# Performance work log

Hardware: AMD Instinct MI355X
Metric: run time of the kernel (lower is better)

## Reference

```python
import jax, jax.numpy as jnp
import numpy as np

IN_DIM = 1024
HID = 1024
DEPTH = 13            # perfect binary tree: 2**13 = 8192 leaves, 8191 internal nodes
N_LEAVES = 2 ** DEPTH
N_TOKENS = 8192
N_OPS = 4             # '+', '/', '*', '-' (ordered_op=False)


def setup_inputs() -> dict:
    key = jax.random.key(0)
    ks = jax.random.split(key, 16)
    sW = 1.0 / np.sqrt(IN_DIM)
    sU = 1.0 / np.sqrt(HID)
    inp = {
        "tokens": jax.random.normal(ks[0], (N_TOKENS, IN_DIM), jnp.float32),
        "leaf_token_ids": jax.random.randint(ks[1], (N_LEAVES,), 0, N_TOKENS),
        "op_ids": jax.random.randint(ks[2], (N_LEAVES - 1,), 0, N_OPS),
        "W_i": jax.random.normal(ks[3], (HID, IN_DIM), jnp.float32) * sW,
        "W_o": jax.random.normal(ks[4], (HID, IN_DIM), jnp.float32) * sW,
        "W_u": jax.random.normal(ks[5], (HID, IN_DIM), jnp.float32) * sW,
        "W_f": jax.random.normal(ks[6], (HID, IN_DIM), jnp.float32) * sW,
        "U_i": jax.random.normal(ks[7], (HID, HID), jnp.float32) * sU,
        "U_o": jax.random.normal(ks[8], (HID, HID), jnp.float32) * sU,
        "U_u": jax.random.normal(ks[9], (HID, HID), jnp.float32) * sU,
        "U_f": jax.random.normal(ks[10], (HID, HID), jnp.float32) * sU,
        "b_i": jnp.zeros((1, HID), jnp.float32),
        "b_o": jnp.zeros((1, HID), jnp.float32),
        "b_u": jnp.zeros((1, HID), jnp.float32),
        "b_f": jnp.zeros((1, HID), jnp.float32),
        "op_emb": jax.random.uniform(ks[11], (N_OPS, IN_DIM), jnp.float32, -1.0, 1.0),
        "c_init": jnp.zeros((2, HID), jnp.float32),
        "h_init": jnp.zeros((2, HID), jnp.float32),
    }
    return inp


def reference(tokens, leaf_token_ids, op_ids, W_i, W_o, W_u, W_f,
              U_i, U_o, U_u, U_f, b_i, b_o, b_u, b_f,
              op_emb, c_init, h_init):
    """Depth-batched Child-Sum TreeLSTM over a perfect binary tree.
    op_ids are stored root-first level order: level l (root=0) occupies
    op_ids[2**l - 1 : 2**(l+1) - 1]. Leaves are level DEPTH.
    Children of node j at level l are nodes 2j, 2j+1 at level l+1.
    Returns jnp.stack([c_root, h_root])  -> [2, 1, HID]."""
    H = U_i.shape[0]

    def node_step(x, c_state, h_state):
        # x: [n, in_dim]; c_state/h_state: [n, 2, H]
        h_sum = h_state.sum(axis=1)                                   # [n, H]
        i = jax.nn.sigmoid(x @ W_i.T + h_sum @ U_i.T + b_i)
        o = jax.nn.sigmoid(x @ W_o.T + h_sum @ U_o.T + b_o)
        u = jnp.tanh(x @ W_u.T + h_sum @ U_u.T + b_u)
        f = jax.nn.sigmoid((x @ W_f.T)[:, None, :] + h_state @ U_f.T + b_f)  # [n,2,H]
        c = i * u + (f * c_state).sum(axis=1)                         # [n, H]
        h = o * jnp.tanh(c)
        return c, h

    n = leaf_token_ids.shape[0]
    depth = int(np.log2(n))
    # leaves: learnable init states, x = embedding of the token
    x = tokens[leaf_token_ids]                                        # [n, in_dim]
    c, h = node_step(x,
                     jnp.broadcast_to(c_init, (n, 2, H)),
                     jnp.broadcast_to(h_init, (n, 2, H)))
    # internal levels, bottom-up
    for l in range(depth - 1, -1, -1):
        m = 2 ** l
        off = m - 1
        x = op_emb[op_ids[off:off + m]]                               # [m, in_dim]
        c, h = node_step(x, c.reshape(m, 2, H), h.reshape(m, 2, H))
    return jnp.stack([c, h])  # [2, 1, H]: root (c, h)
```

## Files before the change

### kernel.cpp

```cpp
#include <hip/hip_runtime.h>

typedef unsigned short u16;
typedef __attribute__((ext_vector_type(4))) unsigned short us4;
typedef __attribute__((ext_vector_type(4))) float f4;
typedef __attribute__((ext_vector_type(8))) short bf16x8;
typedef __attribute__((ext_vector_type(4))) float f32x4;

__device__ __forceinline__ u16 f2bf(float x) {
  unsigned u = __float_as_uint(x);
  return (u16)((u + 0x7FFFu + ((u >> 16) & 1u)) >> 16);
}
__device__ __forceinline__ float b2f(u16 s) {
  return __uint_as_float(((unsigned)s) << 16);
}
__device__ __forceinline__ float sigm(float x) { return 1.f / (1.f + __expf(-x)); }
__device__ __forceinline__ float tanhf_(float x) { return 2.f / (1.f + __expf(-2.f * x)) - 1.f; }

__global__ void convert_wu_kernel(const float* __restrict__ w0, const float* __restrict__ w1,
                                  const float* __restrict__ w2, const float* __restrict__ w3,
                                  const float* __restrict__ u0, const float* __restrict__ u1,
                                  const float* __restrict__ u2, const float* __restrict__ u3,
                                  u16* __restrict__ Wb, u16* __restrict__ Ub) {
  int mat = blockIdx.x >> 10;
  int off4 = (int)(blockIdx.x & 1023) * 256 + threadIdx.x;
  const float* src; u16* dst;
  switch (mat) {
    case 0: src = w0; dst = Wb; break;
    case 1: src = w1; dst = Wb + 1048576; break;
    case 2: src = w2; dst = Wb + 2097152; break;
    case 3: src = w3; dst = Wb + 3145728; break;
    case 4: src = u0; dst = Ub; break;
    case 5: src = u1; dst = Ub + 1048576; break;
    case 6: src = u2; dst = Ub + 2097152; break;
    default: src = u3; dst = Ub + 3145728; break;
  }
  f4 v = ((const f4*)src)[off4];
  us4 o = {f2bf(v[0]), f2bf(v[1]), f2bf(v[2]), f2bf(v[3])};
  ((us4*)dst)[off4] = o;
}

__global__ void gather_leaf_kernel(const float* __restrict__ tokens,
                                   const int* __restrict__ ids, u16* __restrict__ Xl) {
  int n = blockIdx.x, t = threadIdx.x;
  int tok = ids[n];
  f4 v = ((const f4*)(tokens + (size_t)tok * 1024))[t];
  us4 o = {f2bf(v[0]), f2bf(v[1]), f2bf(v[2]), f2bf(v[3])};
  ((us4*)(Xl + (size_t)n * 1024))[t] = o;
}

__global__ void precompute_kernel(const float* __restrict__ op_emb,
    const float* __restrict__ w0, const float* __restrict__ w1,
    const float* __restrict__ w2, const float* __restrict__ w3,
    const float* __restrict__ u0, const float* __restrict__ u1,
    const float* __restrict__ u2, const float* __restrict__ u3,
    const float* __restrict__ b0, const float* __restrict__ b1,
    const float* __restrict__ b2, const float* __restrict__ b3,
    const float* __restrict__ h_init,
    float* __restrict__ xw, float* __restrict__ leafC) {
  int id = blockIdx.x * 256 + threadIdx.x;
  if (id < 16384) {
    int op = id >> 12, g = (id >> 10) & 3, j = id & 1023;
    const float* wsrc; const float* bs;
    switch (g) {
      case 0: wsrc = w0; bs = b0; break;
      case 1: wsrc = w1; bs = b1; break;
      case 2: wsrc = w2; bs = b2; break;
      default: wsrc = w3; bs = b3; break;
    }
    const f4* xr = (const f4*)(op_emb + (size_t)op * 1024);
    const f4* wr = (const f4*)(wsrc + (size_t)j * 1024);
    float s = bs[j];
    for (int k = 0; k < 256; ++k) {
      f4 a = xr[k], b = wr[k];
      s += a[0] * b[0] + a[1] * b[1] + a[2] * b[2] + a[3] * b[3];
    }
    xw[id] = s;
  } else if (id < 21504) {
    int id2 = id - 16384;
    int sel = id2 >> 10, j = id2 & 1023;
    const f4* h0 = (const f4*)h_init;
    const f4* h1 = (const f4*)(h_init + 1024);
    float s;
    if (sel < 3) {
      const float* usrc; const float* bs;
      switch (sel) {
        case 0: usrc = u0; bs = b0; break;
        case 1: usrc = u1; bs = b1; break;
        default: usrc = u2; bs = b2; break;
      }
      const f4* wr = (const f4*)(usrc + (size_t)j * 1024);
      s = bs[j];
      for (int k = 0; k < 256; ++k) {
        f4 a0 = h0[k], a1 = h1[k], b = wr[k];
        s += (a0[0] + a1[0]) * b[0] + (a0[1] + a1[1]) * b[1] +
             (a0[2] + a1[2]) * b[2] + (a0[3] + a1[3]) * b[3];
      }
    } else {
      const f4* hs = (sel == 3) ? h0 : h1;
      const f4* wr = (const f4*)(u3 + (size_t)j * 1024);
      s = b3[j];
      for (int k = 0; k < 256; ++k) {
        f4 a = hs[k], b = wr[k];
        s += a[0] * b[0] + a[1] * b[1] + a[2] * b[2] + a[3] * b[3];
      }
    }
    leafC[id2] = s;
  }
}

template <int NRT, int NCT>
__global__ __launch_bounds__(256, (NRT == 8 ? 2 : 3)) void tree_gemm(
    const u16* __restrict__ A, const u16* __restrict__ Wm,
    const float* __restrict__ consts,
    const int* __restrict__ ops,
    const float* __restrict__ c_in,
    float* __restrict__ c_out, u16* __restrict__ h_out,
    int nrows, int m_parents, int is_leaf, float* __restrict__ out_root) {
  constexpr int ROWS = NRT * 16;
  constexpr int COLS = NCT * 16;
  constexpr int S = 64 / NCT;
  constexpr int LOG2S = (NCT == 2 ? 5 : 4);
  constexpr int NST = NRT / 2;
  constexpr int DBUF = NRT * 2048;
  constexpr int PASSES = (NRT == 8 ? 2 : 1);
  constexpr int RPP = ROWS / PASSES;
  constexpr int FPP = RPP / 16;
  constexpr int SMEM_U16 =
      (4 * RPP * 68 > NRT * 2048 ? 4 * RPP * 68 : NRT * 2048);
  __shared__ __align__(16) u16 smem[SMEM_U16];
  char* smem_c = (char*)smem;

  const int tid = threadIdx.x;
  const int wave = tid >> 6;
  const int lane = tid & 63;
  const int stripe = blockIdx.x & (S - 1);
  const int rowblk = blockIdx.x >> LOG2S;
  const int r0 = rowblk * ROWS;
  const int j0 = stripe * COLS;
  const int ln15 = lane & 15, quad = lane >> 4;
  const int sub = lane >> 3, gsel = lane & 7;

  const char* pAsrc[NST];
  unsigned a_dst[NST];
#pragma unroll
  for (int i = 0; i < NST; ++i) {
    int slot = (wave * NST + i) * 8 + sub;
    int row = r0 + slot; if (row >= nrows) row = nrows - 1;
    pAsrc[i] = (const char*)(A + (size_t)row * 1024 + (unsigned)((gsel ^ sub) * 8));
    a_dst[i] = (unsigned)((wave * NST + i) * 1024 + lane * 16);
  }
  const char* pB[NCT];
#pragma unroll
  for (int f = 0; f < NCT; ++f)
    pB[f] = (const char*)(Wm + (size_t)(wave * 1024 + j0 + f * 16 + ln15) * 1024 + quad * 8);

  unsigned a_base[2];
#pragma unroll
  for (int ks = 0; ks < 2; ++ks)
    a_base[ks] = (unsigned)(ln15 * 128 + (((ks * 4 + quad) ^ (ln15 & 7)) * 16));

  f32x4 acc[NRT][NCT];
#pragma unroll
  for (int t = 0; t < NRT; ++t)
#pragma unroll
    for (int f = 0; f < NCT; ++f) acc[t][f] = (f32x4){0.f, 0.f, 0.f, 0.f};

#pragma unroll
  for (int i = 0; i < NST; ++i)
    __builtin_amdgcn_global_load_lds(
        (const __attribute__((address_space(1))) void*)(pAsrc[i]),
        (__attribute__((address_space(3))) void*)(smem_c + a_dst[i]), 16, 0, 0);
  bf16x8 bcur[2][NCT], bnxt[2][NCT];
#pragma unroll
  for (int ks = 0; ks < 2; ++ks)
#pragma unroll
    for (int f = 0; f < NCT; ++f)
      bcur[ks][f] = *(const bf16x8*)(pB[f] + ks * 64);

#pragma unroll
  for (int ch = 0; ch < 16; ++ch) {
    __syncthreads();
    if (ch < 15) {
#pragma unroll
      for (int i = 0; i < NST; ++i)
        __builtin_amdgcn_global_load_lds(
            (const __attribute__((address_space(1))) void*)(pAsrc[i] + (ch + 1) * 128),
            (__attribute__((address_space(3))) void*)(smem_c + ((ch + 1) & 1) * DBUF + a_dst[i]),
            16, 0, 0);
    }
    const unsigned cb = (unsigned)((ch & 1) * DBUF);
    {
      bf16x8 af[NRT];
#pragma unroll
      for (int t = 0; t < NRT; ++t)
        af[t] = *(const bf16x8*)(smem_c + cb + a_base[0] + t * 2048);
#pragma unroll
      for (int t = 0; t < NRT; ++t)
#pragma unroll
        for (int f = 0; f < NCT; ++f)
          acc[t][f] = __builtin_amdgcn_mfma_f32_16x16x32_bf16(af[t], bcur[0][f],
                                                              acc[t][f], 0, 0, 0);
    }
    if (ch < 15) {
#pragma unroll
      for (int ks = 0; ks < 2; ++ks)
#pragma unroll
        for (int f = 0; f < NCT; ++f)
          bnxt[ks][f] = *(const bf16x8*)(pB[f] + (ch + 1) * 128 + ks * 64);
    }
    {
      bf16x8 af[NRT];
#pragma unroll
      for (int t = 0; t < NRT; ++t)
        af[t] = *(const bf16x8*)(smem_c + cb + a_base[1] + t * 2048);
#pragma unroll
      for (int t = 0; t < NRT; ++t)
#pragma unroll
        for (int f = 0; f < NCT; ++f)
          acc[t][f] = __builtin_amdgcn_mfma_f32_16x16x32_bf16(af[t], bcur[1][f],
                                                              acc[t][f], 0, 0, 0);
    }
#pragma unroll
    for (int ks = 0; ks < 2; ++ks)
#pragma unroll
      for (int f = 0; f < NCT; ++f) bcur[ks][f] = bnxt[ks][f];
  }

#pragma unroll
  for (int pass = 0; pass < PASSES; ++pass) {
    __syncthreads();
#pragma unroll
    for (int tt = 0; tt < FPP; ++tt) {
      int t = pass * FPP + tt;
#pragma unroll
      for (int f = 0; f < NCT; ++f)
#pragma unroll
        for (int k = 0; k < 4; ++k) {
          int row = tt * 16 + quad * 4 + k;
          int col = f * 16 + ln15;
          smem[(wave * RPP + row) * 68 + col] = f2bf(acc[t][f][k]);
        }
    }
    __syncthreads();
    const int rbase = r0 + pass * RPP;

    if (is_leaf) {
      for (int e = tid; e < RPP * COLS; e += 256) {
        int r = e / COLS, j = e % COLS;
        int col = j0 + j, n = rbase + r;
        float p0 = b2f(smem[(0 * RPP + r) * 68 + j]);
        float p1 = b2f(smem[(1 * RPP + r) * 68 + j]);
        float p2 = b2f(smem[(2 * RPP + r) * 68 + j]);
        float p3 = b2f(smem[(3 * RPP + r) * 68 + j]);
        float i_ = sigm(p0 + consts[col]);
        float o_ = sigm(p1 + consts[1024 + col]);
        float u_ = tanhf_(p2 + consts[2048 + col]);
        float f0 = sigm(p3 + consts[3072 + col]);
        float f1 = sigm(p3 + consts[4096 + col]);
        float c = i_ * u_ + f0 * c_in[col] + f1 * c_in[1024 + col];
        float h = o_ * tanhf_(c);
        c_out[(size_t)n * 1024 + col] = c;
        h_out[(size_t)n * 1024 + col] = f2bf(h);
      }
    } else {
      for (int e = tid; e < (RPP / 2) * COLS; e += 256) {
        int p = e / COLS, j = e % COLS;
        int np = (rbase >> 1) + p;
        if (np >= m_parents) break;
        int col = j0 + j;
        int op = ops[np];
        const float* xwop = consts + ((unsigned)(op * 4) << 10);
        float p0a = b2f(smem[(0 * RPP + 2 * p) * 68 + j]), p0b = b2f(smem[(0 * RPP + 2 * p + 1) * 68 + j]);
        float p1a = b2f(smem[(1 * RPP + 2 * p) * 68 + j]), p1b = b2f(smem[(1 * RPP + 2 * p + 1) * 68 + j]);
        float p2a = b2f(smem[(2 * RPP + 2 * p) * 68 + j]), p2b = b2f(smem[(2 * RPP + 2 * p + 1) * 68 + j]);
        float p3a = b2f(smem[(3 * RPP + 2 * p) * 68 + j]), p3b = b2f(smem[(3 * RPP + 2 * p + 1) * 68 + j]);
        float i_ = sigm(p0a + p0b + xwop[col]);
        float o_ = sigm(p1a + p1b + xwop[1024 + col]);
        float u_ = tanhf_(p2a + p2b + xwop[2048 + col]);
        float f0 = sigm(p3a + xwop[3072 + col]);
        float f1 = sigm(p3b + xwop[3072 + col]);
        float c = i_ * u_ + f0 * c_in[(size_t)(rbase + 2 * p) * 1024 + col]
                          + f1 * c_in[(size_t)(rbase + 2 * p + 1) * 1024 + col];
        float h = o_ * tanhf_(c);
        if (m_parents == 1) {
          out_root[col] = c;
          out_root[1024 + col] = h;
        } else {
          c_out[(size_t)np * 1024 + col] = c;
          h_out[(size_t)np * 1024 + col] = f2bf(h);
        }
      }
    }
  }
}

extern "C" void kernel_launch(void* const* d_in, const int* in_sizes, int n_in,
                              void* d_out, int out_size, void* d_ws, size_t ws_size,
                              hipStream_t stream) {
  const float* tokens = (const float*)d_in[0];
  const int* leaf_ids = (const int*)d_in[1];
  const int* op_ids = (const int*)d_in[2];
  const float* W0 = (const float*)d_in[3];
  const float* W1 = (const float*)d_in[4];
  const float* W2 = (const float*)d_in[5];
  const float* W3 = (const float*)d_in[6];
  const float* U0 = (const float*)d_in[7];
  const float* U1 = (const float*)d_in[8];
  const float* U2 = (const float*)d_in[9];
  const float* U3 = (const float*)d_in[10];
  const float* B0 = (const float*)d_in[11];
  const float* B1 = (const float*)d_in[12];
  const float* B2 = (const float*)d_in[13];
  const float* B3 = (const float*)d_in[14];
  const float* op_emb = (const float*)d_in[15];
  const float* c_init = (const float*)d_in[16];
  const float* h_init = (const float*)d_in[17];
  float* out = (float*)d_out;

  char* ws = (char*)d_ws;
  u16* Wb = (u16*)ws;
  u16* Ub = Wb + (size_t)4 * 1024 * 1024;
  u16* Xl = Ub + (size_t)4 * 1024 * 1024;
  u16* hA = Xl + (size_t)8192 * 1024;
  u16* hB = hA + (size_t)8192 * 1024;
  float* cA = (float*)(hB + (size_t)4096 * 1024);
  float* cB = cA + (size_t)8192 * 1024;
  float* xw = cB + (size_t)4096 * 1024;
  float* lc = xw + 16 * 1024;

  convert_wu_kernel<<<8192, 256, 0, stream>>>(W0, W1, W2, W3, U0, U1, U2, U3, Wb, Ub);
  gather_leaf_kernel<<<8192, 256, 0, stream>>>(tokens, leaf_ids, Xl);
  precompute_kernel<<<84, 256, 0, stream>>>(op_emb, W0, W1, W2, W3, U0, U1, U2, U3,
                                            B0, B1, B2, B3, h_init, xw, lc);

  tree_gemm<8, 2><<<64 * 32, 256, 0, stream>>>(Xl, Wb, lc, nullptr, c_init,
                                               cA, hA, 8192, 0, 1, out);

  const u16* hin = hA; const float* cin = cA;
  u16* hout = hB; float* cout = cB;
  for (int l = 12; l >= 0; --l) {
    int m = 1 << l;
    int nrows = 2 * m;
    if (nrows >= 2048) {
      tree_gemm<8, 2><<<(nrows / 128) * 32, 256, 0, stream>>>(
          hin, Ub, xw, op_ids + (m - 1), cin, cout, hout, nrows, m, 0, out);
    } else if (nrows >= 1024) {
      tree_gemm<4, 2><<<(nrows / 64) * 32, 256, 0, stream>>>(
          hin, Ub, xw, op_ids + (m - 1), cin, cout, hout, nrows, m, 0, out);
    } else {
      int rg = nrows / 32; if (rg < 1) rg = 1;
      tree_gemm<2, 2><<<rg * 32, 256, 0, stream>>>(
          hin, Ub, xw, op_ids + (m - 1), cin, cout, hout, nrows, m, 0, out);
    }
    const u16* th = hin; hin = hout; hout = (u16*)th;
    const float* tc = cin; cin = cout; cout = (float*)tc;
  }
}
```

Before: 604.6 us.

## Split internal levels into forget-gate GEMM and child-summed i/o/u GEMM

For the large internal levels (l>=10), the i/o/u gate matmuls now run on the pre-summed child hidden states (h_sum, produced in each epilogue through a lane shuffle). Only the forget gate is computed per child, in a separate fgate_gemm kernel. This roughly halves the FLOPs for three of the four gates, at the cost of an extra kernel launch, extra buffers for the summed h and the f*c partials, and a bf16 rounding of the summed h. The small levels also switch to a new small_gemm kernel that preloads all of A into LDS. The new path is gated on the workspace size.

New measurement: 671.2 us. +11.0%, slower.

```diff
diff --git a/kernel.cpp b/kernel.cpp
--- a/kernel.cpp
+++ b/kernel.cpp
@@ -115,7 +115,8 @@
     const int* __restrict__ ops,
     const float* __restrict__ c_in,
     float* __restrict__ c_out, u16* __restrict__ h_out,
-    int nrows, int m_parents, int is_leaf, float* __restrict__ out_root) {
+    int nrows, int m_parents, int is_leaf, float* __restrict__ out_root,
+    u16* __restrict__ hs_out) {
   constexpr int ROWS = NRT * 16;
   constexpr int COLS = NCT * 16;
   constexpr int S = 64 / NCT;
@@ -261,6 +262,10 @@
         float h = o_ * tanhf_(c);
         c_out[(size_t)n * 1024 + col] = c;
         h_out[(size_t)n * 1024 + col] = f2bf(h);
+        if (hs_out) {
+          float hp = h + __shfl_xor(h, 32);
+          if (lane < 32) hs_out[(size_t)(n >> 1) * 1024 + col] = f2bf(hp);
+        }
       }
     } else {
       for (int e = tid; e < (RPP / 2) * COLS; e += 256) {
@@ -294,6 +299,391 @@
   }
 }
 
+__global__ __launch_bounds__(256, 2) void fgate_gemm(
+    const u16* __restrict__ A, const u16* __restrict__ Uf,
+    const float* __restrict__ xw, const int* __restrict__ ops,
+    const float* __restrict__ c_in, float* __restrict__ fcp,
+    int nrows, int m_parents) {
+  __shared__ __align__(16) u16 smem[16896];
+  char* smem_c = (char*)smem;
+  const int tid = threadIdx.x;
+  const int wave = tid >> 6, lane = tid & 63;
+  const int stripe = blockIdx.x & 7;
+  const int rowblk = blockIdx.x >> 3;
+  const int r0 = rowblk * 128;
+  const int j0 = stripe * 128;
+  const int ln15 = lane & 15, quad = lane >> 4;
+  const int sub = lane >> 3, gsel = lane & 7;
+
+  const char* pAsrc[4];
+  unsigned a_dst[4];
+#pragma unroll
+  for (int i = 0; i < 4; ++i) {
+    int slot = (wave * 4 + i) * 8 + sub;
+    int row = r0 + slot; if (row >= nrows) row = nrows - 1;
+    pAsrc[i] = (const char*)(A + (size_t)row * 1024 + (unsigned)((gsel ^ sub) * 8));
+    a_dst[i] = (unsigned)((wave * 4 + i) * 1024 + lane * 16);
+  }
+  const char* pB[2];
+#pragma unroll
+  for (int f = 0; f < 2; ++f)
+    pB[f] = (const char*)(Uf + (size_t)(j0 + wave * 32 + f * 16 + ln15) * 1024 + quad * 8);
+
+  unsigned a_base[2];
+#pragma unroll
+  for (int ks = 0; ks < 2; ++ks)
+    a_base[ks] = (unsigned)(ln15 * 128 + (((ks * 4 + quad) ^ (ln15 & 7)) * 16));
+
+  f32x4 acc[8][2];
+#pragma unroll
+  for (int t = 0; t < 8; ++t)
+#pragma unroll
+    for (int f = 0; f < 2; ++f) acc[t][f] = (f32x4){0.f, 0.f, 0.f, 0.f};
+
+#pragma unroll
+  for (int i = 0; i < 4; ++i)
+    __builtin_amdgcn_global_load_lds(
+        (const __attribute__((address_space(1))) void*)(pAsrc[i]),
+        (__attribute__((address_space(3))) void*)(smem_c + a_dst[i]), 16, 0, 0);
+  bf16x8 bcur[2][2], bnxt[2][2];
+#pragma unroll
+  for (int ks = 0; ks < 2; ++ks)
+#pragma unroll
+    for (int f = 0; f < 2; ++f)
+      bcur[ks][f] = *(const bf16x8*)(pB[f] + ks * 64);
+
+#pragma unroll
+  for (int ch = 0; ch < 16; ++ch) {
+    __syncthreads();
+    if (ch < 15) {
+#pragma unroll
+      for (int i = 0; i < 4; ++i)
+        __builtin_amdgcn_global_load_lds(
+            (const __attribute__((address_space(1))) void*)(pAsrc[i] + (ch + 1) * 128),
+            (__attribute__((address_space(3))) void*)(smem_c + ((ch + 1) & 1) * 16384 + a_dst[i]),
+            16, 0, 0);
+    }
+    const unsigned cb = (unsigned)((ch & 1) * 16384);
+    {
+      bf16x8 af[8];
+#pragma unroll
+      for (int t = 0; t < 8; ++t)
+        af[t] = *(const bf16x8*)(smem_c + cb + a_base[0] + t * 2048);
+#pragma unroll
+      for (int t = 0; t < 8; ++t)
+#pragma unroll
+        for (int f = 0; f < 2; ++f)
+          acc[t][f] = __builtin_amdgcn_mfma_f32_16x16x32_bf16(af[t], bcur[0][f],
+                                                              acc[t][f], 0, 0, 0);
+    }
+    if (ch < 15) {
+#pragma unroll
+      for (int ks = 0; ks < 2; ++ks)
+#pragma unroll
+        for (int f = 0; f < 2; ++f)
+          bnxt[ks][f] = *(const bf16x8*)(pB[f] + (ch + 1) * 128 + ks * 64);
+    }
+    {
+      bf16x8 af[8];
+#pragma unroll
+      for (int t = 0; t < 8; ++t)
+        af[t] = *(const bf16x8*)(smem_c + cb + a_base[1] + t * 2048);
+#pragma unroll
+      for (int t = 0; t < 8; ++t)
+#pragma unroll
+        for (int f = 0; f < 2; ++f)
+          acc[t][f] = __builtin_amdgcn_mfma_f32_16x16x32_bf16(af[t], bcur[1][f],
+                                                              acc[t][f], 0, 0, 0);
+    }
+#pragma unroll
+    for (int ks = 0; ks < 2; ++ks)
+#pragma unroll
+      for (int f = 0; f < 2; ++f) bcur[ks][f] = bnxt[ks][f];
+  }
+
+  __syncthreads();
+#pragma unroll
+  for (int t = 0; t < 8; ++t)
+#pragma unroll
+    for (int f = 0; f < 2; ++f)
+#pragma unroll
+      for (int k = 0; k < 4; ++k) {
+        int row = t * 16 + quad * 4 + k;
+        int col = wave * 32 + f * 16 + ln15;
+        smem[row * 132 + col] = f2bf(acc[t][f][k]);
+      }
+  __syncthreads();
+  for (int e = tid; e < 64 * 128; e += 256) {
+    int p = e >> 7, j = e & 127;
+    int q = (r0 >> 1) + p;
+    if (q >= m_parents) break;
+    int col = j0 + j;
+    int op = ops[q];
+    float xwf = xw[((unsigned)op << 12) + 3072u + (unsigned)col];
+    float f0 = sigm(b2f(smem[(2 * p) * 132 + j]) + xwf);
+    float f1 = sigm(b2f(smem[(2 * p + 1) * 132 + j]) + xwf);
+    fcp[(size_t)q * 1024 + col] = f0 * c_in[(size_t)(r0 + 2 * p) * 1024 + col]
+                                + f1 * c_in[(size_t)(r0 + 2 * p + 1) * 1024 + col];
+  }
+}
+
+__global__ __launch_bounds__(192, 2) void sum3_gemm(
+    const u16* __restrict__ A, const u16* __restrict__ Um,
+    const float* __restrict__ xw, const int* __restrict__ ops,
+    const float* __restrict__ fc,
+    float* __restrict__ c_out, u16* __restrict__ h_out,
+    u16* __restrict__ hs_out, int m_rows) {
+  __shared__ __align__(16) u16 smem[16384];
+  char* smem_c = (char*)smem;
+  const int tid = threadIdx.x;
+  const int wave = tid >> 6, lane = tid & 63;
+  const int stripe = blockIdx.x & 31;
+  const int rowblk = blockIdx.x >> 5;
+  const int r0 = rowblk * 128;
+  const int j0 = stripe * 32;
+  const int ln15 = lane & 15, quad = lane >> 4;
+  const int sub = lane >> 3, gsel = lane & 7;
+
+  const char* pAs[6];
+  unsigned adst[6];
+  int nj = 0;
+#pragma unroll
+  for (int i = 0; i < 6; ++i) {
+    int w = wave + i * 3;
+    if (w < 16) {
+      int row = r0 + w * 8 + sub;
+      if (row >= m_rows) row = m_rows - 1;
+      pAs[i] = (const char*)(A + (size_t)row * 1024 + (unsigned)((gsel ^ sub) * 8));
+      adst[i] = (unsigned)(w * 1024 + lane * 16);
+      nj = i + 1;
+    }
+  }
+  const char* pB[2];
+#pragma unroll
+  for (int f = 0; f < 2; ++f)
+    pB[f] = (const char*)(Um + ((size_t)wave << 20) + (size_t)(j0 + f * 16 + ln15) * 1024 + quad * 8);
+
+  unsigned a_base[2];
+#pragma unroll
+  for (int ks = 0; ks < 2; ++ks)
+    a_base[ks] = (unsigned)(ln15 * 128 + (((ks * 4 + quad) ^ (ln15 & 7)) * 16));
+
+  f32x4 acc[8][2];
+#pragma unroll
+  for (int t = 0; t < 8; ++t)
+#pragma unroll
+    for (int f = 0; f < 2; ++f) acc[t][f] = (f32x4){0.f, 0.f, 0.f, 0.f};
+
+#pragma unroll
+  for (int i = 0; i < 6; ++i)
+    if (i < nj)
+      __builtin_amdgcn_global_load_lds(
+          (const __attribute__((address_space(1))) void*)(pAs[i]),
+          (__attribute__((address_space(3))) void*)(smem_c + adst[i]), 16, 0, 0);
+  bf16x8 bcur[2][2], bnxt[2][2];
+#pragma unroll
+  for (int ks = 0; ks < 2; ++ks)
+#pragma unroll
+    for (int f = 0; f < 2; ++f)
+      bcur[ks][f] = *(const bf16x8*)(pB[f] + ks * 64);
+
+#pragma unroll
+  for (int ch = 0; ch < 16; ++ch) {
+    __syncthreads();
+    if (ch < 15) {
+#pragma unroll
+      for (int i = 0; i < 6; ++i)
+        if (i < nj)
+          __builtin_amdgcn_global_load_lds(
+              (const __attribute__((address_space(1))) void*)(pAs[i] + (ch + 1) * 128),
+              (__attribute__((address_space(3))) void*)(smem_c + ((ch + 1) & 1) * 16384 + adst[i]),
+              16, 0, 0);
+    }
+    const unsigned cb = (unsigned)((ch & 1) * 16384);
+    {
+      bf16x8 af[8];
+#pragma unroll
+      for (int t = 0; t < 8; ++t)
+        af[t] = *(const bf16x8*)(smem_c + cb + a_base[0] + t * 2048);
+#pragma unroll
+      for (int t = 0; t < 8; ++t)
+#pragma unroll
+        for (int f = 0; f < 2; ++f)
+          acc[t][f] = __builtin_amdgcn_mfma_f32_16x16x32_bf16(af[t], bcur[0][f],
+                                                              acc[t][f], 0, 0, 0);
+    }
+    if (ch < 15) {
+#pragma unroll
+      for (int ks = 0; ks < 2; ++ks)
+#pragma unroll
+        for (int f = 0; f < 2; ++f)
+          bnxt[ks][f] = *(const bf16x8*)(pB[f] + (ch + 1) * 128 + ks * 64);
+    }
+    {
+      bf16x8 af[8];
+#pragma unroll
+      for (int t = 0; t < 8; ++t)
+        af[t] = *(const bf16x8*)(smem_c + cb + a_base[1] + t * 2048);
+#pragma unroll
+      for (int t = 0; t < 8; ++t)
+#pragma unroll
+        for (int f = 0; f < 2; ++f)
+          acc[t][f] = __builtin_amdgcn_mfma_f32_16x16x32_bf16(af[t], bcur[1][f],
+                                                              acc[t][f], 0, 0, 0);
+    }
+#pragma unroll
+    for (int ks = 0; ks < 2; ++ks)
+#pragma unroll
+      for (int f = 0; f < 2; ++f) bcur[ks][f] = bnxt[ks][f];
+  }
+
+#pragma unroll
+  for (int pass = 0; pass < 2; ++pass) {
+    __syncthreads();
+#pragma unroll
+    for (int tt = 0; tt < 4; ++tt) {
+      int t = pass * 4 + tt;
+#pragma unroll
+      for (int f = 0; f < 2; ++f)
+#pragma unroll
+        for (int k = 0; k < 4; ++k) {
+          int row = tt * 16 + quad * 4 + k;
+          int col = f * 16 + ln15;
+          smem[(wave * 64 + row) * 68 + col] = f2bf(acc[t][f][k]);
+        }
+    }
+    __syncthreads();
+    const int rbase = r0 + pass * 64;
+    for (int e = tid; e < 64 * 32; e += 192) {
+      int r = e >> 5, j = e & 31;
+      int p = rbase + r;
+      int col = j0 + j;
+      int op = ops[p];
+      const float* xwop = xw + ((unsigned)op << 12);
+      float g0 = b2f(smem[(0 * 64 + r) * 68 + j]);
+      float g1 = b2f(smem[(1 * 64 + r) * 68 + j]);
+      float g2 = b2f(smem[(2 * 64 + r) * 68 + j]);
+      float i_ = sigm(g0 + xwop[col]);
+      float o_ = sigm(g1 + xwop[1024 + col]);
+      float u_ = tanhf_(g2 + xwop[2048 + col]);
+      float c = i_ * u_ + fc[(size_t)p * 1024 + col];
+      float h = o_ * tanhf_(c);
+      c_out[(size_t)p * 1024 + col] = c;
+      h_out[(size_t)p * 1024 + col] = f2bf(h);
+      if (hs_out) {
+        float hp = h + __shfl_xor(h, 32);
+        if (lane < 32) hs_out[(size_t)(p >> 1) * 1024 + col] = f2bf(hp);
+      }
+    }
+  }
+}
+
+__global__ __launch_bounds__(256, 2) void small_gemm(
+    const u16* __restrict__ A, const u16* __restrict__ Um,
+    const float* __restrict__ xw, const int* __restrict__ ops,
+    const float* __restrict__ c_in,
+    float* __restrict__ c_out, u16* __restrict__ h_out,
+    int nrows, int m_parents, float* __restrict__ out_root) {
+  __shared__ __align__(16) u16 smem[32768];
+  char* smem_c = (char*)smem;
+  const int tid = threadIdx.x;
+  const int wave = tid >> 6, lane = tid & 63;
+  const int stripe = blockIdx.x & 31, rowblk = blockIdx.x >> 5;
+  const int r0 = rowblk * 32, j0 = stripe * 32;
+  const int ln15 = lane & 15, quad = lane >> 4;
+  const int sub = lane >> 3, gsel = lane & 7;
+
+#pragma unroll
+  for (int i = 0; i < 16; ++i) {
+    int w = wave * 16 + i;
+    int ch = w >> 2;
+    int row = r0 + (w & 3) * 8 + sub;
+    if (row >= nrows) row = nrows - 1;
+    const char* src = (const char*)(A + (size_t)row * 1024 + (unsigned)(ch * 64) + (unsigned)((gsel ^ sub) * 8));
+    __builtin_amdgcn_global_load_lds(
+        (const __attribute__((address_space(1))) void*)src,
+        (__attribute__((address_space(3))) void*)(smem_c + w * 1024 + lane * 16), 16, 0, 0);
+  }
+  const char* pB[2];
+#pragma unroll
+  for (int f = 0; f < 2; ++f)
+    pB[f] = (const char*)(Um + (size_t)(wave * 1024 + j0 + f * 16 + ln15) * 1024 + quad * 8);
+  unsigned a_base[2];
+#pragma unroll
+  for (int ks = 0; ks < 2; ++ks)
+    a_base[ks] = (unsigned)(ln15 * 128 + (((ks * 4 + quad) ^ (ln15 & 7)) * 16));
+
+  f32x4 acc[2][2];
+#pragma unroll
+  for (int t = 0; t < 2; ++t)
+#pragma unroll
+    for (int f = 0; f < 2; ++f) acc[t][f] = (f32x4){0.f, 0.f, 0.f, 0.f};
+
+  __syncthreads();
+
+#pragma unroll
+  for (int ch = 0; ch < 16; ++ch) {
+    bf16x8 b[2][2];
+#pragma unroll
+    for (int ks = 0; ks < 2; ++ks)
+#pragma unroll
+      for (int f = 0; f < 2; ++f)
+        b[ks][f] = *(const bf16x8*)(pB[f] + ch * 128 + ks * 64);
+#pragma unroll
+    for (int ks = 0; ks < 2; ++ks) {
+      bf16x8 af[2];
+#pragma unroll
+      for (int t = 0; t < 2; ++t)
+        af[t] = *(const bf16x8*)(smem_c + ch * 4096 + a_base[ks] + t * 2048);
+#pragma unroll
+      for (int t = 0; t < 2; ++t)
+#pragma unroll
+        for (int f = 0; f < 2; ++f)
+          acc[t][f] = __builtin_amdgcn_mfma_f32_16x16x32_bf16(af[t], b[ks][f], acc[t][f], 0, 0, 0);
+    }
+  }
+
+  __syncthreads();
+#pragma unroll
+  for (int t = 0; t < 2; ++t)
+#pragma unroll
+    for (int f = 0; f < 2; ++f)
+#pragma unroll
+      for (int k = 0; k < 4; ++k) {
+        int row = t * 16 + quad * 4 + k;
+        int col = f * 16 + ln15;
+        smem[(wave * 32 + row) * 68 + col] = f2bf(acc[t][f][k]);
+      }
+  __syncthreads();
+  for (int e = tid; e < 16 * 32; e += 256) {
+    int p = e >> 5, j = e & 31;
+    int np = (r0 >> 1) + p;
+    if (np >= m_parents) break;
+    int col = j0 + j;
+    int op = ops[np];
+    const float* xwop = xw + ((unsigned)op << 12);
+    float p0a = b2f(smem[(0 * 32 + 2 * p) * 68 + j]), p0b = b2f(smem[(0 * 32 + 2 * p + 1) * 68 + j]);
+    float p1a = b2f(smem[(1 * 32 + 2 * p) * 68 + j]), p1b = b2f(smem[(1 * 32 + 2 * p + 1) * 68 + j]);
+    float p2a = b2f(smem[(2 * 32 + 2 * p) * 68 + j]), p2b = b2f(smem[(2 * 32 + 2 * p + 1) * 68 + j]);
+    float p3a = b2f(smem[(3 * 32 + 2 * p) * 68 + j]), p3b = b2f(smem[(3 * 32 + 2 * p + 1) * 68 + j]);
+    float i_ = sigm(p0a + p0b + xwop[col]);
+    float o_ = sigm(p1a + p1b + xwop[1024 + col]);
+    float u_ = tanhf_(p2a + p2b + xwop[2048 + col]);
+    float f0 = sigm(p3a + xwop[3072 + col]);
+    float f1 = sigm(p3b + xwop[3072 + col]);
+    float c = i_ * u_ + f0 * c_in[(size_t)(r0 + 2 * p) * 1024 + col]
+                      + f1 * c_in[(size_t)(r0 + 2 * p + 1) * 1024 + col];
+    float h = o_ * tanhf_(c);
+    if (m_parents == 1) {
+      out_root[col] = c;
+      out_root[1024 + col] = h;
+    } else {
+      c_out[(size_t)np * 1024 + col] = c;
+      h_out[(size_t)np * 1024 + col] = f2bf(h);
+    }
+  }
+}
+
 extern "C" void kernel_launch(void* const* d_in, const int* in_sizes, int n_in,
                               void* d_out, int out_size, void* d_ws, size_t ws_size,
                               hipStream_t stream) {
@@ -327,6 +717,10 @@
   float* cB = cA + (size_t)8192 * 1024;
   float* xw = cB + (size_t)4096 * 1024;
   float* lc = xw + 16 * 1024;
+  const bool split_ok = ws_size >= (size_t)118 * 1024 * 1024;
+  u16* hsA = (u16*)(ws + (size_t)105 * 1024 * 1024);
+  u16* hsB = (u16*)(ws + (size_t)113 * 1024 * 1024);
+  float* fc = (float*)Xl;
 
   convert_wu_kernel<<<8192, 256, 0, stream>>>(W0, W1, W2, W3, U0, U1, U2, U3, Wb, Ub);
   gather_leaf_kernel<<<8192, 256, 0, stream>>>(tokens, leaf_ids, Xl);
@@ -334,23 +728,32 @@
                                             B0, B1, B2, B3, h_init, xw, lc);
 
   tree_gemm<8, 2><<<64 * 32, 256, 0, stream>>>(Xl, Wb, lc, nullptr, c_init,
-                                               cA, hA, 8192, 0, 1, out);
+                                               cA, hA, 8192, 0, 1, out,
+                                               split_ok ? hsA : nullptr);
 
   const u16* hin = hA; const float* cin = cA;
   u16* hout = hB; float* cout = cB;
+  u16* hs_cur = hsA; u16* hs_nxt = hsB;
   for (int l = 12; l >= 0; --l) {
     int m = 1 << l;
     int nrows = 2 * m;
-    if (nrows >= 2048) {
+    if (l >= 10 && split_ok) {
+      fgate_gemm<<<(nrows / 128) * 8, 256, 0, stream>>>(
+          hin, Ub + (size_t)3 * 1048576, xw, op_ids + (m - 1), cin, fc, nrows, m);
+      sum3_gemm<<<(m / 128) * 32, 192, 0, stream>>>(
+          hs_cur, Ub, xw, op_ids + (m - 1), fc, cout, hout,
+          (l > 10) ? hs_nxt : nullptr, m);
+      u16* th = hs_cur; hs_cur = hs_nxt; hs_nxt = th;
+    } else if (nrows >= 2048) {
       tree_gemm<8, 2><<<(nrows / 128) * 32, 256, 0, stream>>>(
-          hin, Ub, xw, op_ids + (m - 1), cin, cout, hout, nrows, m, 0, out);
+          hin, Ub, xw, op_ids + (m - 1), cin, cout, hout, nrows, m, 0, out, nullptr);
     } else if (nrows >= 1024) {
       tree_gemm<4, 2><<<(nrows / 64) * 32, 256, 0, stream>>>(
-          hin, Ub, xw, op_ids + (m - 1), cin, cout, hout, nrows, m, 0, out);
+          hin, Ub, xw, op_ids + (m - 1), cin, cout, hout, nrows, m, 0, out, nullptr);
     } else {
       int rg = nrows / 32; if (rg < 1) rg = 1;
-      tree_gemm<2, 2><<<rg * 32, 256, 0, stream>>>(
-          hin, Ub, xw, op_ids + (m - 1), cin, cout, hout, nrows, m, 0, out);
+      small_gemm<<<rg * 32, 256, 0, stream>>>(
+          hin, Ub, xw, op_ids + (m - 1), cin, cout, hout, nrows, m, out);
     }
     const u16* th = hin; hin = hout; hout = (u16*)th;
     const float* tc = cin; cin = cout; cout = (float*)tc;
```

## Fuse top tree levels into one persistent kernel with grid barriers

Applied to the files above, without the earlier changes.

Levels 8 through 0 of the tree were each a separate small GEMM launch. They are replaced by a single persistent kernel of 256 blocks that loops over the levels. Software grid barriers built on global atomics separate the levels, and the h/c buffers ping-pong between them. This removes per-launch overhead and idle gaps on the latency-bound top of the tree. It relies on all blocks being co-resident and on a workspace size check, falling back to the old launch loop if the workspace is too small.

Result: slower. 934.8 us (+54.6%).

```diff
diff --git a/kernel.cpp b/kernel.cpp
--- a/kernel.cpp
+++ b/kernel.cpp
@@ -294,6 +294,149 @@
   }
 }
 
+__device__ __forceinline__ void grid_bar(int* bar) {
+  __syncthreads();
+  if (threadIdx.x == 0) {
+    __threadfence();
+    int v = __hip_atomic_fetch_add(&bar[0], 1, __ATOMIC_ACQ_REL, __HIP_MEMORY_SCOPE_AGENT);
+    if (v == 255) {
+      __hip_atomic_store(&bar[1], 1, __ATOMIC_RELEASE, __HIP_MEMORY_SCOPE_AGENT);
+    } else {
+      while (!__hip_atomic_load(&bar[1], __ATOMIC_ACQUIRE, __HIP_MEMORY_SCOPE_AGENT))
+        __builtin_amdgcn_s_sleep(8);
+    }
+    __threadfence();
+  }
+  __syncthreads();
+}
+
+__global__ __launch_bounds__(256, 1) void tail_kernel(
+    const u16* __restrict__ h9, const float* __restrict__ c9,
+    u16* __restrict__ hW0, float* __restrict__ cW0,
+    u16* __restrict__ hW1, float* __restrict__ cW1,
+    const u16* __restrict__ Um, const float* __restrict__ xw,
+    const int* __restrict__ op_ids, int* __restrict__ bar,
+    float* __restrict__ out_root) {
+  __shared__ __align__(16) u16 smem[32768];
+  char* smem_c = (char*)smem;
+  const int tid = threadIdx.x;
+  const int wave = tid >> 6, lane = tid & 63;
+  const int ln15 = lane & 15, quad = lane >> 4;
+  const int sub = lane >> 3, gsel = lane & 7;
+  unsigned a_base[2];
+#pragma unroll
+  for (int ks = 0; ks < 2; ++ks)
+    a_base[ks] = (unsigned)(ln15 * 128 + (((ks * 4 + quad) ^ (ln15 & 7)) * 16));
+
+  const u16* hin = h9; const float* cin = c9;
+  u16* hw = hW0; float* cw = cW0;
+  u16* hx = hW1; float* cx = cW1;
+
+  for (int l = 8; l >= 0; --l) {
+    const int m = 1 << l;
+    const int nrows = 2 * m;
+    const int* ops = op_ids + (m - 1);
+    const int rg = (nrows + 31) >> 5;
+    const int J = rg << 5;
+    for (int job = blockIdx.x; job < J; job += 256) {
+      const int rowblk = job >> 5, stripe = job & 31;
+      const int r0 = rowblk * 32, j0 = stripe * 32;
+      __syncthreads();
+#pragma unroll
+      for (int i = 0; i < 16; ++i) {
+        int w = wave * 16 + i;
+        int ch = w >> 2;
+        int row = r0 + (w & 3) * 8 + sub;
+        if (row >= nrows) row = nrows - 1;
+        const u16* src = hin + (size_t)row * 1024 + (unsigned)(ch * 64) + (unsigned)((gsel ^ sub) * 8);
+        __builtin_amdgcn_global_load_lds(
+            (const __attribute__((address_space(1))) void*)src,
+            (__attribute__((address_space(3))) void*)(smem_c + w * 1024 + lane * 16), 16, 0, 0);
+      }
+      const char* pB[2];
+#pragma unroll
+      for (int f = 0; f < 2; ++f)
+        pB[f] = (const char*)(Um + (size_t)(wave * 1024 + j0 + f * 16 + ln15) * 1024 + quad * 8);
+
+      f32x4 acc[2][2];
+#pragma unroll
+      for (int t = 0; t < 2; ++t)
+#pragma unroll
+        for (int f = 0; f < 2; ++f) acc[t][f] = (f32x4){0.f, 0.f, 0.f, 0.f};
+
+      __syncthreads();
+
+#pragma unroll
+      for (int ch = 0; ch < 16; ++ch) {
+        bf16x8 b[2][2];
+#pragma unroll
+        for (int ks = 0; ks < 2; ++ks)
+#pragma unroll
+          for (int f = 0; f < 2; ++f)
+            b[ks][f] = *(const bf16x8*)(pB[f] + ch * 128 + ks * 64);
+#pragma unroll
+        for (int ks = 0; ks < 2; ++ks) {
+          bf16x8 af[2];
+#pragma unroll
+          for (int t = 0; t < 2; ++t)
+            af[t] = *(const bf16x8*)(smem_c + ch * 4096 + a_base[ks] + t * 2048);
+#pragma unroll
+          for (int t = 0; t < 2; ++t)
+#pragma unroll
+            for (int f = 0; f < 2; ++f)
+              acc[t][f] = __builtin_amdgcn_mfma_f32_16x16x32_bf16(af[t], b[ks][f], acc[t][f], 0, 0, 0);
+        }
+      }
+
+      __syncthreads();
+#pragma unroll
+      for (int t = 0; t < 2; ++t)
+#pragma unroll
+        for (int f = 0; f < 2; ++f)
+#pragma unroll
+          for (int k = 0; k < 4; ++k) {
+            int row = t * 16 + quad * 4 + k;
+            int col = f * 16 + ln15;
+            smem[(wave * 32 + row) * 68 + col] = f2bf(acc[t][f][k]);
+          }
+      __syncthreads();
+      for (int e = tid; e < 16 * 32; e += 256) {
+        int p = e >> 5, j = e & 31;
+        int np = (r0 >> 1) + p;
+        if (np >= m) break;
+        int col = j0 + j;
+        int op = ops[np];
+        const float* xwop = xw + ((unsigned)op << 12);
+        float p0a = b2f(smem[(0 * 32 + 2 * p) * 68 + j]), p0b = b2f(smem[(0 * 32 + 2 * p + 1) * 68 + j]);
+        float p1a = b2f(smem[(1 * 32 + 2 * p) * 68 + j]), p1b = b2f(smem[(1 * 32 + 2 * p + 1) * 68 + j]);
+        float p2a = b2f(smem[(2 * 32 + 2 * p) * 68 + j]), p2b = b2f(smem[(2 * 32 + 2 * p + 1) * 68 + j]);
+        float p3a = b2f(smem[(3 * 32 + 2 * p) * 68 + j]), p3b = b2f(smem[(3 * 32 + 2 * p + 1) * 68 + j]);
+        float i_ = sigm(p0a + p0b + xwop[col]);
+        float o_ = sigm(p1a + p1b + xwop[1024 + col]);
+        float u_ = tanhf_(p2a + p2b + xwop[2048 + col]);
+        float f0 = sigm(p3a + xwop[3072 + col]);
+        float f1 = sigm(p3b + xwop[3072 + col]);
+        float c = i_ * u_ + f0 * cin[(size_t)(r0 + 2 * p) * 1024 + col]
+                          + f1 * cin[(size_t)(r0 + 2 * p + 1) * 1024 + col];
+        float h = o_ * tanhf_(c);
+        if (m == 1) {
+          out_root[col] = c;
+          out_root[1024 + col] = h;
+        } else {
+          cw[(size_t)np * 1024 + col] = c;
+          hw[(size_t)np * 1024 + col] = f2bf(h);
+        }
+      }
+    }
+    if (l > 0) {
+      grid_bar(bar + (8 - l) * 2);
+      hin = hw; cin = cw;
+      u16* th = hx; hx = hw; hw = th;
+      float* tc = cx; cx = cw; cw = tc;
+    }
+  }
+}
+
 extern "C" void kernel_launch(void* const* d_in, const int* in_sizes, int n_in,
                               void* d_out, int out_size, void* d_ws, size_t ws_size,
                               hipStream_t stream) {
@@ -327,6 +470,8 @@
   float* cB = cA + (size_t)8192 * 1024;
   float* xw = cB + (size_t)4096 * 1024;
   float* lc = xw + 16 * 1024;
+  int* bar = (int*)(ws + (size_t)110 * 1024 * 1024);
+  const bool tail_ok = ws_size >= (size_t)111 * 1024 * 1024;
 
   convert_wu_kernel<<<8192, 256, 0, stream>>>(W0, W1, W2, W3, U0, U1, U2, U3, Wb, Ub);
   gather_leaf_kernel<<<8192, 256, 0, stream>>>(tokens, leaf_ids, Xl);
@@ -336,23 +481,35 @@
   tree_gemm<8, 2><<<64 * 32, 256, 0, stream>>>(Xl, Wb, lc, nullptr, c_init,
                                                cA, hA, 8192, 0, 1, out);
 
-  const u16* hin = hA; const float* cin = cA;
+  u16* hin = hA; float* cin = cA;
   u16* hout = hB; float* cout = cB;
-  for (int l = 12; l >= 0; --l) {
+  for (int l = 12; l >= 9; --l) {
     int m = 1 << l;
     int nrows = 2 * m;
     if (nrows >= 2048) {
       tree_gemm<8, 2><<<(nrows / 128) * 32, 256, 0, stream>>>(
           hin, Ub, xw, op_ids + (m - 1), cin, cout, hout, nrows, m, 0, out);
-    } else if (nrows >= 1024) {
+    } else {
       tree_gemm<4, 2><<<(nrows / 64) * 32, 256, 0, stream>>>(
           hin, Ub, xw, op_ids + (m - 1), cin, cout, hout, nrows, m, 0, out);
-    } else {
+    }
+    u16* th = hin; hin = hout; hout = th;
+    float* tc = cin; cin = cout; cout = tc;
+  }
+
+  if (tail_ok) {
+    hipMemsetAsync(bar, 0, 256, stream);
+    tail_kernel<<<256, 256, 0, stream>>>(hin, cin, hout, cout, hin, cin,
+                                         Ub, xw, op_ids, bar, out);
+  } else {
+    for (int l = 8; l >= 0; --l) {
+      int m = 1 << l;
+      int nrows = 2 * m;
       int rg = nrows / 32; if (rg < 1) rg = 1;
       tree_gemm<2, 2><<<rg * 32, 256, 0, stream>>>(
           hin, Ub, xw, op_ids + (m - 1), cin, cout, hout, nrows, m, 0, out);
-    }
-    const u16* th = hin; hin = hout; hout = (u16*)th;
-    const float* tc = cin; cin = cout; cout = (float*)tc;
-  }
-}
+      u16* th = hin; hin = hout; hout = th;
+      float* tc = cin; cin = cout; cout = tc;
+    }
+  }
+}
```
